# Performance work log

Hardware: AMD Instinct MI355X
Metric: run time of the kernel (lower is better)

## Reference

```python
import jax, jax.numpy as jnp
import numpy as np
import math

B, K, T = 4, 1024, 2048
OD, H = 128, 8


def setup_inputs() -> dict:
    key = jax.random.key(0)
    ks = jax.random.split(key, 6)
    s_in = 1.0 / math.sqrt(K)
    s_u = 1.0 / math.sqrt(H * OD)
    return {
        "x": jax.random.normal(ks[0], (B, K, T), dtype=jnp.float32),
        "Wk": jax.random.uniform(ks[1], (H * OD, K), minval=-s_in, maxval=s_in, dtype=jnp.float32),
        "Wq": jax.random.uniform(ks[2], (H * OD, K), minval=-s_in, maxval=s_in, dtype=jnp.float32),
        "Wv": jax.random.uniform(ks[3], (H * OD, K), minval=-s_in, maxval=s_in, dtype=jnp.float32),
        "Wu": jax.random.uniform(ks[4], (OD, H * OD), minval=-s_u, maxval=s_u, dtype=jnp.float32),
        "bu": jax.random.uniform(ks[5], (OD,), minval=-s_u, maxval=s_u, dtype=jnp.float32),
    }


def reference(x, Wk, Wq, Wv, Wu, bu):
    b, k, t = x.shape
    # QKV projections: Linear applied over channel dim of channels-first input
    keys = jnp.einsum('bkt,jk->bjt', x, Wk).reshape(b, H, OD, t)
    queries = jnp.einsum('bkt,jk->bjt', x, Wq).reshape(b, H, OD, t)
    values = jnp.einsum('bkt,jk->bjt', x, Wv).reshape(b, H, OD, t)
    # attention scores over time: [b, h, t, t]
    dot = jnp.einsum('bhkt,bhki->bhti', queries, keys) / math.sqrt(OD)
    dot = jax.nn.softmax(dot, axis=-1)
    out = jnp.einsum('bhti,bhki->bhkt', dot, values)  # [b, h, od, t]
    # unify heads: weight (OD, H*OD) viewed as (OD_out=k, H=h, OD=e)
    out = jnp.einsum('bhet,khe->bkt', out, Wu.reshape(OD, H, OD))
    return out + bu[None, :, None]
```

## Files before the change

kernel.cpp:

```cpp
#include <hip/hip_runtime.h>
#include <hip/hip_bf16.h>
#include <type_traits>
#include <utility>

#define DEVINL __device__ __forceinline__

typedef unsigned short u16;
typedef unsigned int   u32;
typedef short  s8v __attribute__((ext_vector_type(8)));
typedef __bf16 b8v __attribute__((ext_vector_type(8)));
typedef float  f4v __attribute__((ext_vector_type(4)));

static constexpr int BB = 4, KD = 1024, TT = 2048, OD = 128, NH = 8;
static constexpr int J2 = 2048;

template<class V, class = void> struct mfma_takes : std::false_type {};
template<class V> struct mfma_takes<V, std::void_t<decltype(
    __builtin_amdgcn_mfma_f32_16x16x32_bf16(std::declval<V>(), std::declval<V>(),
                                            std::declval<f4v>(), 0, 0, 0))>> : std::true_type {};

template<class AV>
DEVINL f4v mfma16(AV a, AV b, f4v c) {
  if constexpr (mfma_takes<AV>::value) {
    return __builtin_amdgcn_mfma_f32_16x16x32_bf16(a, b, c, 0, 0, 0);
  } else {
    return __builtin_amdgcn_mfma_f32_16x16x32_bf16(
        __builtin_bit_cast(b8v, a), __builtin_bit_cast(b8v, b), c, 0, 0, 0);
  }
}

DEVINL u16 f2bf(float f) {
  union { float f; u32 u; } v; v.f = f;
  u32 u = v.u;
  return (u16)((u + 0x7fffu + ((u >> 16) & 1u)) >> 16);
}
DEVINL float bf2f(u16 h) { union { u32 u; float f; } v; v.u = ((u32)h) << 16; return v.f; }

DEVINL u32 cvtpk_bf16(float a, float b) {
  u32 r;
  asm("v_cvt_pk_bf16_f32 %0, %1, %2" : "=v"(r) : "v"(a), "v"(b));
  return r;
}

DEVINL void gload_lds16(const void* g, void* l) {
  __builtin_amdgcn_global_load_lds(
      (const __attribute__((address_space(1))) void*)g,
      (__attribute__((address_space(3))) void*)l, 16, 0, 0);
}

__global__ void xpose_split_x(const float* __restrict__ x, u16* __restrict__ xTh) {
  __shared__ float tile[32][33];
  const int b  = blockIdx.z;
  const int k0 = blockIdx.y * 32;
  const int t0 = blockIdx.x * 32;
  const int tx = threadIdx.x;
  const int ty = threadIdx.y;
  const float* xb = x + (size_t)b * KD * TT;
#pragma unroll
  for (int j = 0; j < 4; ++j)
    tile[ty + j * 8][tx] = xb[(size_t)(k0 + ty + j * 8) * TT + t0 + tx];
  __syncthreads();
  u16* oh = xTh + (size_t)b * TT * KD;
#pragma unroll
  for (int j = 0; j < 4; ++j) {
    int t = ty + j * 8;
    float v = tile[tx][t];
    oh[(size_t)(t0 + t) * KD + k0 + tx] = f2bf(v);
  }
}

__global__ void split_weights(const float* __restrict__ Wk, const float* __restrict__ Wq,
                              const float* __restrict__ Wv, const float* __restrict__ Wu,
                              u16* __restrict__ Wkqh, u16* __restrict__ Wvh,
                              u16* __restrict__ Wuh,  u16* __restrict__ Wul,
                              float qscale) {
  int i = blockIdx.x * 256 + threadIdx.x;
  if (i < 1048576) {
    Wkqh[i] = f2bf(Wk[i]);
    Wkqh[1048576 + i] = f2bf(Wq[i] * qscale);
    Wvh[i] = f2bf(Wv[i]);
    if (i < 131072) {
      float v = Wu[i];  u16 hh = f2bf(v);
      Wuh[i] = hh;      Wul[i] = f2bf(v - bf2f(hh));
    }
  }
}

template<int EPI>
__global__ __launch_bounds__(256, 3) void gemm_bt_split(
    const u16* __restrict__ Ahi, const u16* __restrict__ Alo,
    const u16* __restrict__ Bhi, const u16* __restrict__ Blo,
    void* __restrict__ Couth,
    const float* __restrict__ bias,
    int Kdim, int ldc, long strideA, long strideB, long strideC, int npass) {
  __shared__ __align__(16) u16 At[128 * 64];
  __shared__ __align__(16) u16 Bt[128 * 64];
  const int tid = threadIdx.x;
  const int w = tid >> 6, l = tid & 63;
  const int wm = w >> 1, wn = w & 1;
  const int lr = l & 15, lg = l >> 4;
  const int b = blockIdx.z;
  const u16* Ah = Ahi + (size_t)b * strideA;
  const u16* Al = Alo ? Alo + (size_t)b * strideA : nullptr;
  const u16* Bh = Bhi + (size_t)b * strideB;
  const u16* Bl = Blo ? Blo + (size_t)b * strideB : nullptr;
  const int m0 = blockIdx.x * 128;
  const int n0 = (EPI == 3) ? ((blockIdx.y & 15) * 128) : (blockIdx.y * 128);
  const int ky = (EPI == 3) ? (blockIdx.y >> 4) : 0;
  const int kspan = (EPI == 3) ? (Kdim / 2) : Kdim;
  const int kbase = ky * kspan;

  int srow[4], soff[4];
#pragma unroll
  for (int i = 0; i < 4; ++i) {
    int c = tid + i * 256;
    int row = c >> 3, q = c & 7;
    srow[i] = row;
    soff[i] = (q ^ (row & 7)) * 8;
  }

  f4v acc[4][4] = {};

  const int spi = kspan / 64;
  const int iters = npass * spi;
  for (int it = 0; it < iters; ++it) {
    const int seg = it / spi;
    const int k = kbase + (it - seg * spi) * 64;
    const u16* As = (seg == 2) ? Al : Ah;
    const u16* Bs = (seg == 1) ? Bl : Bh;
#pragma unroll
    for (int i = 0; i < 4; ++i) {
      int c = tid + i * 256;
      gload_lds16(As + (size_t)(m0 + srow[i]) * Kdim + k + soff[i], (char*)At + c * 16);
      gload_lds16(Bs + (size_t)(n0 + srow[i]) * Kdim + k + soff[i], (char*)Bt + c * 16);
    }
    __syncthreads();
    __builtin_amdgcn_s_setprio(1);
#pragma unroll
    for (int kk = 0; kk < 2; ++kk) {
      const int q = kk * 4 + lg;
      s8v a[4], bb[4];
#pragma unroll
      for (int mi = 0; mi < 4; ++mi) {
        int row = wm * 64 + mi * 16 + lr;
        a[mi] = *(const s8v*)(&At[row * 64 + (q ^ (row & 7)) * 8]);
      }
#pragma unroll
      for (int ni = 0; ni < 4; ++ni) {
        int row = wn * 64 + ni * 16 + lr;
        bb[ni] = *(const s8v*)(&Bt[row * 64 + (q ^ (row & 7)) * 8]);
      }
#pragma unroll
      for (int mi = 0; mi < 4; ++mi)
#pragma unroll
        for (int ni = 0; ni < 4; ++ni)
          acc[mi][ni] = mfma16(a[mi], bb[ni], acc[mi][ni]);
    }
    __builtin_amdgcn_s_setprio(0);
    __syncthreads();
  }

  if constexpr (EPI == 2) {
    u16* Ch = (u16*)Couth + (size_t)b * strideC;
#pragma unroll
    for (int mi = 0; mi < 4; ++mi)
#pragma unroll
      for (int ni = 0; ni < 4; ++ni)
#pragma unroll
        for (int r = 0; r < 4; ++r) {
          int m = m0 + wm * 64 + mi * 16 + lg * 4 + r;
          int n = n0 + wn * 64 + ni * 16 + lr;
          Ch[(size_t)m * ldc + n] = f2bf(acc[mi][ni][r]);
        }
  } else if constexpr (EPI == 3) {
    float* C = (float*)Couth + ((size_t)ky * BB + b) * strideC;
#pragma unroll
    for (int mi = 0; mi < 4; ++mi)
#pragma unroll
      for (int ni = 0; ni < 4; ++ni)
#pragma unroll
        for (int r = 0; r < 4; ++r) {
          int m = m0 + wm * 64 + mi * 16 + lg * 4 + r;
          int n = n0 + wn * 64 + ni * 16 + lr;
          C[(size_t)m * ldc + n] = acc[mi][ni][r];
        }
  } else {
    float* C = (float*)Couth + (size_t)b * strideC;
#pragma unroll
    for (int mi = 0; mi < 4; ++mi)
#pragma unroll
      for (int ni = 0; ni < 4; ++ni)
#pragma unroll
        for (int r = 0; r < 4; ++r) {
          int m = m0 + wm * 64 + mi * 16 + lg * 4 + r;
          int n = n0 + wn * 64 + ni * 16 + lr;
          C[(size_t)m * ldc + n] = acc[mi][ni][r] + bias[m];
        }
  }
}

__global__ void addbias(const float* __restrict__ part, float* __restrict__ out,
                        const float* __restrict__ bias) {
  int i = blockIdx.x * 256 + threadIdx.x;
  f4v a = ((const f4v*)part)[i];
  f4v c = ((const f4v*)part)[i + 262144];
  float bs = bias[(i >> 9) & 127];
  f4v r;
#pragma unroll
  for (int j = 0; j < 4; ++j) r[j] = a[j] + c[j] + bs;
  ((f4v*)out)[i] = r;
}

__global__ __launch_bounds__(512, 4) void attn_fwd(
    const u16* __restrict__ QKTh, const u16* __restrict__ Vh,
    u16* __restrict__ OTh, u16* __restrict__ OTl) {
  __shared__ __align__(16) u16 Ksh[2][64 * 128];
  __shared__ __align__(16) u16 Vsh[2][128 * 64];
  __shared__ __align__(16) u16 Ph[128 * 64];

  const int bid = blockIdx.x;
  const int lid = (bid & 7) * 64 + (bid >> 3);
  const int t0 = (lid & 15) * 128;
  const int h  = (lid >> 4) & 7;
  const int b  = lid >> 7;

  const int tid = threadIdx.x;
  const int w = tid >> 6, l = tid & 63;
  const int lr = l & 15, lg = l >> 4;
  const size_t qb = (size_t)b * TT * J2;
  const u16* Qh_ = QKTh + qb + 1024 + h * 128;
  const u16* Kh_ = QKTh + qb + h * 128;
  const u16* Vh_ = Vh + (size_t)b * 1024 * TT + (size_t)h * 128 * TT;

  int koff[2], kdo[2], voff[2], vdo[2];
#pragma unroll
  for (int i = 0; i < 2; ++i) {
    int c = tid + i * 512;
    { int row = c >> 4, q = c & 15;
      koff[i] = row * J2 + (q ^ (row & 7)) * 8;  kdo[i] = c * 16; }
    { int row = c >> 3, q = c & 7;
      voff[i] = row * TT + (q ^ (row & 7)) * 8;  vdo[i] = c * 16; }
  }

#define ATTN_STAGE(BSEL, I0) do {                                          \
    _Pragma("unroll")                                                      \
    for (int i_ = 0; i_ < 2; ++i_) {                                       \
      gload_lds16(Kh_ + (size_t)(I0) * J2 + koff[i_], (char*)Ksh[BSEL] + kdo[i_]); \
      gload_lds16(Vh_ + voff[i_] + (I0),              (char*)Vsh[BSEL] + vdo[i_]); \
    } } while (0)

  s8v qh[4];
  {
    const size_t trow = (size_t)(t0 + w * 16 + lr) * J2;
#pragma unroll
    for (int kk = 0; kk < 4; ++kk)
      qh[kk] = *(const s8v*)(Qh_ + trow + kk * 32 + lg * 8);
  }

  char* Pw = (char*)Ph + w * 16 * 128;
  const int pswz = (lr & 7) << 4;

  f4v o[8] = {};
  float mrow = -1e30f, lsum = 0.f;

  ATTN_STAGE(0, 0);

  for (int it = 0; it < 32; ++it) {
    const int cur = it & 1;
    if (it + 1 < 32) {
      ATTN_STAGE(cur ^ 1, (it + 1) * 64);
      asm volatile("s_waitcnt vmcnt(4)" ::: "memory");
    } else {
      asm volatile("s_waitcnt vmcnt(0)" ::: "memory");
    }
    __builtin_amdgcn_s_barrier();

    const u16* Ks = Ksh[cur];
    const u16* Vs = Vsh[cur];
    f4v s[4] = {};
    __builtin_amdgcn_s_setprio(1);
#pragma unroll
    for (int ni = 0; ni < 4; ++ni) {
      const int row = ni * 16 + lr;
      const int rx = row & 7;
#pragma unroll
      for (int kk = 0; kk < 4; ++kk) {
        const int q = kk * 4 + lg;
        s8v kh = *(const s8v*)(&Ks[row * 128 + (q ^ rx) * 8]);
        s[ni] = mfma16(kh, qh[kk], s[ni]);
      }
    }
    __builtin_amdgcn_s_setprio(0);

    float smax = fmaxf(fmaxf(s[0][0], s[0][1]), fmaxf(s[0][2], s[0][3]));
#pragma unroll
    for (int ni = 1; ni < 4; ++ni)
      smax = fmaxf(smax, fmaxf(fmaxf(s[ni][0], s[ni][1]), fmaxf(s[ni][2], s[ni][3])));
    smax = fmaxf(smax, __shfl_xor(smax, 16));
    smax = fmaxf(smax, __shfl_xor(smax, 32));

    if (__any(smax > mrow + 8.0f)) {
      float mn = fmaxf(mrow, smax);
      float al = exp2f(mrow - mn);
      mrow = mn;
      lsum *= al;
#pragma unroll
      for (int r = 0; r < 4; ++r) {
        float ar = __shfl(al, (l & 48) + ((l >> 4) << 2) + r);
#pragma unroll
        for (int et = 0; et < 8; ++et) o[et][r] *= ar;
      }
    }

    float p[4][4];
    float rsum = 0.f;
#pragma unroll
    for (int ni = 0; ni < 4; ++ni)
#pragma unroll
      for (int r = 0; r < 4; ++r) {
        float pv = exp2f(s[ni][r] - mrow);
        p[ni][r] = pv;
        rsum += pv;
      }
    rsum += __shfl_xor(rsum, 16);
    rsum += __shfl_xor(rsum, 32);
    lsum += rsum;

#pragma unroll
    for (int ni = 0; ni < 4; ++ni) {
      uint2 t;
      t.x = cvtpk_bf16(p[ni][0], p[ni][1]);
      t.y = cvtpk_bf16(p[ni][2], p[ni][3]);
      *(uint2*)(Pw + ((lr * 128 + ni * 32 + lg * 8) ^ pswz)) = t;
    }
    asm volatile("" ::: "memory");
    __builtin_amdgcn_sched_barrier(0);

    __builtin_amdgcn_s_setprio(1);
#pragma unroll
    for (int kk = 0; kk < 2; ++kk) {
      s8v pa = *(const s8v*)(Pw + ((lr * 128 + kk * 64 + lg * 16) ^ pswz));
#pragma unroll
      for (int et = 0; et < 8; ++et) {
        const int vrow = et * 16 + lr;
        s8v vh = *(const s8v*)(&Vs[vrow * 64 + ((kk * 4 + lg) ^ (vrow & 7)) * 8]);
        o[et] = mfma16(pa, vh, o[et]);
      }
    }
    __builtin_amdgcn_s_setprio(0);
    if (it + 1 < 32)
      __builtin_amdgcn_s_barrier();
  }
#undef ATTN_STAGE

  u16* oh = OTh + (size_t)b * TT * 1024;
  u16* ol = OTl + (size_t)b * TT * 1024;
#pragma unroll
  for (int r = 0; r < 4; ++r) {
    float ls = __shfl(lsum, (l & 48) + ((l >> 4) << 2) + r);
    float inv = 1.0f / ls;
    int t = t0 + w * 16 + lg * 4 + r;
#pragma unroll
    for (int et = 0; et < 8; ++et) {
      int he = h * 128 + et * 16 + lr;
      float v = o[et][r] * inv;
      u16 hh = f2bf(v);
      oh[(size_t)t * 1024 + he] = hh;
      ol[(size_t)t * 1024 + he] = f2bf(v - bf2f(hh));
    }
  }
}

extern "C" void kernel_launch(void* const* d_in, const int* in_sizes, int n_in,
                              void* d_out, int out_size, void* d_ws, size_t ws_size,
                              hipStream_t stream) {
  const float* x  = (const float*)d_in[0];
  const float* Wk = (const float*)d_in[1];
  const float* Wq = (const float*)d_in[2];
  const float* Wv = (const float*)d_in[3];
  const float* Wu = (const float*)d_in[4];
  const float* bu = (const float*)d_in[5];
  float* out = (float*)d_out;

  const size_t need_bytes = 2ull * (8388608ull + 2097152ull + 1048576ull +
                                    131072ull * 2 + 16777216ull + 8388608ull +
                                    8388608ull * 2 + 4194304ull);
  if (ws_size < need_bytes) {
    hipMemsetAsync(d_out, 0, (size_t)out_size * sizeof(float), stream);
    return;
  }
  u16* p = (u16*)d_ws;
  u16* xTh = p;  p += 8388608;
  u16* Wkqh = p; p += 2097152;
  u16* Wvh = p;  p += 1048576;
  u16* Wuh = p;  p += 131072;
  u16* Wul = p;  p += 131072;
  u16* QKTh = p; p += 16777216;
  u16* Vh = p;   p += 8388608;
  u16* OTh = p;  p += 8388608;
  u16* OTl = p;  p += 8388608;
  float* Cpart = (float*)p; p += 4194304;

  const float qscale = 0.08838834764831845f * 1.4426950408889634f;

  xpose_split_x<<<dim3(64, 32, 4), dim3(32, 8), 0, stream>>>(x, xTh);
  split_weights<<<4096, 256, 0, stream>>>(Wk, Wq, Wv, Wu, Wkqh, Wvh, Wuh, Wul, qscale);

  gemm_bt_split<2><<<dim3(16, 16, 4), 256, 0, stream>>>(
      xTh, nullptr, Wkqh, nullptr, QKTh, nullptr,
      1024, 2048, 2097152L, 0L, 4194304L, 1);
  gemm_bt_split<2><<<dim3(8, 16, 4), 256, 0, stream>>>(
      Wvh, nullptr, xTh, nullptr, Vh, nullptr,
      1024, 2048, 0L, 2097152L, 2097152L, 1);
  attn_fwd<<<dim3(512), dim3(512), 0, stream>>>(QKTh, Vh, OTh, OTl);
  gemm_bt_split<3><<<dim3(1, 32, 4), 256, 0, stream>>>(
      Wuh, Wul, OTh, OTl, Cpart, nullptr,
      1024, 2048, 0L, 2097152L, 262144L, 3);
  addbias<<<1024, 256, 0, stream>>>(Cpart, out, bu);
}
```

Measured before the change: 203.9 us.

## Switch attention kernel to 32x32x16 MFMA with 4 waves of 32 query rows

The flash-attention kernel now uses 32x32x16 bf16 MFMA instead of 16x16x32. Each of 4 waves (256 threads) handles 32 query rows instead of 16 rows across 8 waves, so each wave keeps more accumulator state and K/V fragments are reused more per LDS read. Load offsets, P-buffer layout, softmax reductions and the output indexing are rewritten for the 32x32 accumulator layout. In exchange there are fewer waves per block and more registers per wave, which may reduce the ability to hide latency.

```diff
diff --git a/kernel.cpp b/kernel.cpp
--- a/kernel.cpp
+++ b/kernel.cpp
@@ -7,9 +7,10 @@
 
 typedef unsigned short u16;
 typedef unsigned int   u32;
-typedef short  s8v __attribute__((ext_vector_type(8)));
-typedef __bf16 b8v __attribute__((ext_vector_type(8)));
-typedef float  f4v __attribute__((ext_vector_type(4)));
+typedef short  s8v  __attribute__((ext_vector_type(8)));
+typedef __bf16 b8v  __attribute__((ext_vector_type(8)));
+typedef float  f4v  __attribute__((ext_vector_type(4)));
+typedef float  f16v __attribute__((ext_vector_type(16)));
 
 static constexpr int BB = 4, KD = 1024, TT = 2048, OD = 128, NH = 8;
 static constexpr int J2 = 2048;
@@ -25,6 +26,21 @@
     return __builtin_amdgcn_mfma_f32_16x16x32_bf16(a, b, c, 0, 0, 0);
   } else {
     return __builtin_amdgcn_mfma_f32_16x16x32_bf16(
+        __builtin_bit_cast(b8v, a), __builtin_bit_cast(b8v, b), c, 0, 0, 0);
+  }
+}
+
+template<class V, class = void> struct mfma32_takes : std::false_type {};
+template<class V> struct mfma32_takes<V, std::void_t<decltype(
+    __builtin_amdgcn_mfma_f32_32x32x16_bf16(std::declval<V>(), std::declval<V>(),
+                                            std::declval<f16v>(), 0, 0, 0))>> : std::true_type {};
+
+template<class AV>
+DEVINL f16v mfma32(AV a, AV b, f16v c) {
+  if constexpr (mfma32_takes<AV>::value) {
+    return __builtin_amdgcn_mfma_f32_32x32x16_bf16(a, b, c, 0, 0, 0);
+  } else {
+    return __builtin_amdgcn_mfma_f32_32x32x16_bf16(
         __builtin_bit_cast(b8v, a), __builtin_bit_cast(b8v, b), c, 0, 0, 0);
   }
 }
@@ -211,7 +227,7 @@
   ((f4v*)out)[i] = r;
 }
 
-__global__ __launch_bounds__(512, 4) void attn_fwd(
+__global__ __launch_bounds__(256, 2) void attn_fwd(
     const u16* __restrict__ QKTh, const u16* __restrict__ Vh,
     u16* __restrict__ OTh, u16* __restrict__ OTl) {
   __shared__ __align__(16) u16 Ksh[2][64 * 128];
@@ -226,16 +242,16 @@
 
   const int tid = threadIdx.x;
   const int w = tid >> 6, l = tid & 63;
-  const int lr = l & 15, lg = l >> 4;
+  const int lw = l & 31, hi = l >> 5;
   const size_t qb = (size_t)b * TT * J2;
   const u16* Qh_ = QKTh + qb + 1024 + h * 128;
   const u16* Kh_ = QKTh + qb + h * 128;
   const u16* Vh_ = Vh + (size_t)b * 1024 * TT + (size_t)h * 128 * TT;
 
-  int koff[2], kdo[2], voff[2], vdo[2];
-#pragma unroll
-  for (int i = 0; i < 2; ++i) {
-    int c = tid + i * 512;
+  int koff[4], kdo[4], voff[4], vdo[4];
+#pragma unroll
+  for (int i = 0; i < 4; ++i) {
+    int c = tid + i * 256;
     { int row = c >> 4, q = c & 15;
       koff[i] = row * J2 + (q ^ (row & 7)) * 8;  kdo[i] = c * 16; }
     { int row = c >> 3, q = c & 7;
@@ -244,23 +260,23 @@
 
 #define ATTN_STAGE(BSEL, I0) do {                                          \
     _Pragma("unroll")                                                      \
-    for (int i_ = 0; i_ < 2; ++i_) {                                       \
+    for (int i_ = 0; i_ < 4; ++i_) {                                       \
       gload_lds16(Kh_ + (size_t)(I0) * J2 + koff[i_], (char*)Ksh[BSEL] + kdo[i_]); \
       gload_lds16(Vh_ + voff[i_] + (I0),              (char*)Vsh[BSEL] + vdo[i_]); \
     } } while (0)
 
-  s8v qh[4];
+  s8v qh[8];
   {
-    const size_t trow = (size_t)(t0 + w * 16 + lr) * J2;
-#pragma unroll
-    for (int kk = 0; kk < 4; ++kk)
-      qh[kk] = *(const s8v*)(Qh_ + trow + kk * 32 + lg * 8);
-  }
-
-  char* Pw = (char*)Ph + w * 16 * 128;
-  const int pswz = (lr & 7) << 4;
-
-  f4v o[8] = {};
+    const size_t trow = (size_t)(t0 + w * 32 + lw) * J2;
+#pragma unroll
+    for (int st = 0; st < 8; ++st)
+      qh[st] = *(const s8v*)(Qh_ + trow + st * 16 + hi * 8);
+  }
+
+  const int prow = (w * 32 + lw) * 128;
+  const int pswz = (lw & 7) << 4;
+
+  f16v o[4] = {};
   float mrow = -1e30f, lsum = 0.f;
 
   ATTN_STAGE(0, 0);
@@ -269,7 +285,7 @@
     const int cur = it & 1;
     if (it + 1 < 32) {
       ATTN_STAGE(cur ^ 1, (it + 1) * 64);
-      asm volatile("s_waitcnt vmcnt(4)" ::: "memory");
+      asm volatile("s_waitcnt vmcnt(8)" ::: "memory");
     } else {
       asm volatile("s_waitcnt vmcnt(0)" ::: "memory");
     }
@@ -277,26 +293,23 @@
 
     const u16* Ks = Ksh[cur];
     const u16* Vs = Vsh[cur];
-    f4v s[4] = {};
+    f16v s[2] = {};
     __builtin_amdgcn_s_setprio(1);
 #pragma unroll
-    for (int ni = 0; ni < 4; ++ni) {
-      const int row = ni * 16 + lr;
-      const int rx = row & 7;
-#pragma unroll
-      for (int kk = 0; kk < 4; ++kk) {
-        const int q = kk * 4 + lg;
-        s8v kh = *(const s8v*)(&Ks[row * 128 + (q ^ rx) * 8]);
-        s[ni] = mfma16(kh, qh[kk], s[ni]);
-      }
+    for (int st = 0; st < 8; ++st) {
+      const int sl = ((st * 2 + hi) ^ (lw & 7)) * 8;
+      s8v k0 = *(const s8v*)(&Ks[lw * 128 + sl]);
+      s8v k1 = *(const s8v*)(&Ks[(32 + lw) * 128 + sl]);
+      s[0] = mfma32(k0, qh[st], s[0]);
+      s[1] = mfma32(k1, qh[st], s[1]);
     }
     __builtin_amdgcn_s_setprio(0);
 
-    float smax = fmaxf(fmaxf(s[0][0], s[0][1]), fmaxf(s[0][2], s[0][3]));
-#pragma unroll
-    for (int ni = 1; ni < 4; ++ni)
-      smax = fmaxf(smax, fmaxf(fmaxf(s[ni][0], s[ni][1]), fmaxf(s[ni][2], s[ni][3])));
-    smax = fmaxf(smax, __shfl_xor(smax, 16));
+    float smax = s[0][0];
+#pragma unroll
+    for (int r = 1; r < 16; ++r) smax = fmaxf(smax, s[0][r]);
+#pragma unroll
+    for (int r = 0; r < 16; ++r) smax = fmaxf(smax, s[1][r]);
     smax = fmaxf(smax, __shfl_xor(smax, 32));
 
     if (__any(smax > mrow + 8.0f)) {
@@ -305,46 +318,44 @@
       mrow = mn;
       lsum *= al;
 #pragma unroll
-      for (int r = 0; r < 4; ++r) {
-        float ar = __shfl(al, (l & 48) + ((l >> 4) << 2) + r);
-#pragma unroll
-        for (int et = 0; et < 8; ++et) o[et][r] *= ar;
+      for (int r = 0; r < 16; ++r) {
+        float ar = __shfl(al, (r & 3) + 8 * (r >> 2) + 4 * hi);
+#pragma unroll
+        for (int et = 0; et < 4; ++et) o[et][r] *= ar;
       }
     }
 
-    float p[4][4];
+    float p0[16], p1[16];
     float rsum = 0.f;
 #pragma unroll
-    for (int ni = 0; ni < 4; ++ni)
-#pragma unroll
-      for (int r = 0; r < 4; ++r) {
-        float pv = exp2f(s[ni][r] - mrow);
-        p[ni][r] = pv;
-        rsum += pv;
-      }
-    rsum += __shfl_xor(rsum, 16);
+    for (int r = 0; r < 16; ++r) { p0[r] = exp2f(s[0][r] - mrow); rsum += p0[r]; }
+#pragma unroll
+    for (int r = 0; r < 16; ++r) { p1[r] = exp2f(s[1][r] - mrow); rsum += p1[r]; }
     rsum += __shfl_xor(rsum, 32);
     lsum += rsum;
 
 #pragma unroll
-    for (int ni = 0; ni < 4; ++ni) {
-      uint2 t;
-      t.x = cvtpk_bf16(p[ni][0], p[ni][1]);
-      t.y = cvtpk_bf16(p[ni][2], p[ni][3]);
-      *(uint2*)(Pw + ((lr * 128 + ni * 32 + lg * 8) ^ pswz)) = t;
+    for (int g = 0; g < 4; ++g) {
+      uint2 ta, tb;
+      ta.x = cvtpk_bf16(p0[g * 4 + 0], p0[g * 4 + 1]);
+      ta.y = cvtpk_bf16(p0[g * 4 + 2], p0[g * 4 + 3]);
+      *(uint2*)((char*)Ph + prow + ((g * 16 + hi * 8) ^ pswz)) = ta;
+      tb.x = cvtpk_bf16(p1[g * 4 + 0], p1[g * 4 + 1]);
+      tb.y = cvtpk_bf16(p1[g * 4 + 2], p1[g * 4 + 3]);
+      *(uint2*)((char*)Ph + prow + ((64 + g * 16 + hi * 8) ^ pswz)) = tb;
     }
     asm volatile("" ::: "memory");
     __builtin_amdgcn_sched_barrier(0);
 
     __builtin_amdgcn_s_setprio(1);
 #pragma unroll
-    for (int kk = 0; kk < 2; ++kk) {
-      s8v pa = *(const s8v*)(Pw + ((lr * 128 + kk * 64 + lg * 16) ^ pswz));
-#pragma unroll
-      for (int et = 0; et < 8; ++et) {
-        const int vrow = et * 16 + lr;
-        s8v vh = *(const s8v*)(&Vs[vrow * 64 + ((kk * 4 + lg) ^ (vrow & 7)) * 8]);
-        o[et] = mfma16(pa, vh, o[et]);
+    for (int ks = 0; ks < 4; ++ks) {
+      s8v pa = *(const s8v*)((char*)Ph + prow + (((ks * 2 + hi) * 16) ^ pswz));
+#pragma unroll
+      for (int et = 0; et < 4; ++et) {
+        const int vrow = et * 32 + lw;
+        s8v vh = *(const s8v*)(&Vs[vrow * 64 + (((ks * 2 + hi) ^ (lw & 7)) * 8)]);
+        o[et] = mfma32(pa, vh, o[et]);
       }
     }
     __builtin_amdgcn_s_setprio(0);
@@ -356,13 +367,14 @@
   u16* oh = OTh + (size_t)b * TT * 1024;
   u16* ol = OTl + (size_t)b * TT * 1024;
 #pragma unroll
-  for (int r = 0; r < 4; ++r) {
-    float ls = __shfl(lsum, (l & 48) + ((l >> 4) << 2) + r);
+  for (int r = 0; r < 16; ++r) {
+    const int qrow = (r & 3) + 8 * (r >> 2) + 4 * hi;
+    float ls = __shfl(lsum, qrow);
     float inv = 1.0f / ls;
-    int t = t0 + w * 16 + lg * 4 + r;
-#pragma unroll
-    for (int et = 0; et < 8; ++et) {
-      int he = h * 128 + et * 16 + lr;
+    int t = t0 + w * 32 + qrow;
+#pragma unroll
+    for (int et = 0; et < 4; ++et) {
+      int he = h * 128 + et * 32 + lw;
       float v = o[et][r] * inv;
       u16 hh = f2bf(v);
       oh[(size_t)t * 1024 + he] = hh;
@@ -412,7 +424,7 @@
   gemm_bt_split<2><<<dim3(8, 16, 4), 256, 0, stream>>>(
       Wvh, nullptr, xTh, nullptr, Vh, nullptr,
       1024, 2048, 0L, 2097152L, 2097152L, 1);
-  attn_fwd<<<dim3(512), dim3(512), 0, stream>>>(QKTh, Vh, OTh, OTl);
+  attn_fwd<<<dim3(512), dim3(256), 0, stream>>>(QKTh, Vh, OTh, OTl);
   gemm_bt_split<3><<<dim3(1, 32, 4), 256, 0, stream>>>(
       Wuh, Wul, OTh, OTl, Cpart, nullptr,
       1024, 2048, 0L, 2097152L, 262144L, 3);
```

Result: no change. 200.4 us (-1.7%).
